# Kernel optimization log

Hardware: AMD Instinct MI355X
Metric: run time of the kernel (lower is better)

Reference implementation:

```python
import jax, jax.numpy as jnp
import numpy as np

B, S, D, H = 4, 2048, 1024, 16
DK = D // H


def setup_inputs() -> dict:
    key = jax.random.key(0)
    ks = jax.random.split(key, 12)
    s = 1.0 / np.sqrt(D)
    return {
        "query": jax.random.normal(ks[0], (B, S, D), jnp.float32),
        "key": jax.random.normal(ks[1], (B, S, D), jnp.float32),
        "value": jax.random.normal(ks[2], (B, S, D), jnp.float32),
        "mask": jnp.ones((1, 1, S, S), jnp.int32),
        "w_q": jax.random.normal(ks[3], (D, D), jnp.float32) * s,
        "b_q": jax.random.normal(ks[4], (D,), jnp.float32) * s,
        "w_k": jax.random.normal(ks[5], (D, D), jnp.float32) * s,
        "b_k": jax.random.normal(ks[6], (D,), jnp.float32) * s,
        "w_v": jax.random.normal(ks[7], (D, D), jnp.float32) * s,
        "b_v": jax.random.normal(ks[8], (D,), jnp.float32) * s,
        "w_o": jax.random.normal(ks[9], (D, D), jnp.float32) * s,
        "b_o": jax.random.normal(ks[10], (D,), jnp.float32) * s,
    }


def reference(query, key, value, mask, w_q, b_q, w_k, b_k, w_v, b_v, w_o, b_o):
    # linear projections (torch Linear: x @ W^T + b)
    q = query @ w_q.T + b_q
    k = key @ w_k.T + b_k
    v = value @ w_v.T + b_v
    # [B, S, D] -> [B, H, S, DK]
    q = q.reshape(B, S, H, DK).transpose(0, 2, 1, 3)
    k = k.reshape(B, S, H, DK).transpose(0, 2, 1, 3)
    v = v.reshape(B, S, H, DK).transpose(0, 2, 1, 3)
    scores = jnp.einsum("bhqd,bhkd->bhqk", q, k) / jnp.sqrt(jnp.float32(DK))
    scores = jnp.where(mask == 0, jnp.float32(-1e9), scores)
    attn = jax.nn.softmax(scores, axis=-1)  # dropout p=0.0 -> identity
    x = jnp.einsum("bhqk,bhkd->bhqd", attn, v)
    x = x.transpose(0, 2, 1, 3).reshape(B, S, D)
    return x @ w_o.T + b_o
```

## Files before the change

### kernel.cpp

```cpp
#include <hip/hip_runtime.h>
#include <stdint.h>

#define S_LEN 2048
#define NHEAD 16
#define DHEAD 64
#define DMODEL 1024
#define MROWS 8192

typedef unsigned short ushort_t;
typedef __attribute__((ext_vector_type(8))) __bf16 bf16x8;
typedef __attribute__((ext_vector_type(4))) float f32x4;

__device__ __forceinline__ float bf2f(ushort_t h) {
    union { unsigned int u; float f; } v; v.u = ((unsigned int)h) << 16; return v.f;
}
__device__ __forceinline__ ushort_t f2bf(float f) {
    union { float f; unsigned int u; } v; v.f = f;
    unsigned int u = v.u + 0x7fffu + ((v.u >> 16) & 1u);
    return (ushort_t)(u >> 16);
}

__device__ __forceinline__ void gload_lds16(const void* g, void* l)
{
    auto* g1 = reinterpret_cast<const __attribute__((address_space(1))) void*>(
        reinterpret_cast<uintptr_t>(g));
    auto* l3 = reinterpret_cast<__attribute__((address_space(3))) void*>(
        reinterpret_cast<uintptr_t>(l));
    __builtin_amdgcn_global_load_lds(g1, l3, 16, 0, 0);
}

__global__ void detect_dtype(const unsigned int* __restrict__ q, int* __restrict__ flag)
{
    __shared__ int cnt;
    if (threadIdx.x == 0) cnt = 0;
    __syncthreads();
    int c = 0;
    for (int i = 0; i < 8; ++i) {
        const unsigned int w = q[threadIdx.x * 8 + i];
        const unsigned int lo = w & 0xffffu;
        const unsigned int e = (lo >> 7) & 0xffu;
        if (lo == 0u || (e >= 96u && e <= 160u)) ++c;
    }
    atomicAdd(&cnt, c);
    __syncthreads();
    if (threadIdx.x == 0) flag[0] = (cnt < 400) ? 1 : 0;
}

__global__ void mask_flags(const int* __restrict__ mask, int* __restrict__ flags)
{
    __shared__ int ok_s;
    if (threadIdx.x == 0) ok_s = 1;
    __syncthreads();
    const int t = blockIdx.x;
    const int tq = t >> 4, tk = t & 15;
    int ok = 1;
    for (int i = 0; i < 64; ++i) {
        const int idx = i * 256 + threadIdx.x;
        const int r = idx >> 7, c = idx & 127;
        if (mask[(size_t)(tq * 128 + r) * S_LEN + tk * 128 + c] == 0) { ok = 0; break; }
    }
    if (!ok) atomicAnd(&ok_s, 0);
    __syncthreads();
    if (threadIdx.x == 0) flags[t] = ok_s;
}

__device__ __forceinline__ float loadscal(const void* b, int i, bool f32)
{
    return f32 ? ((const float*)b)[i] : bf2f(((const ushort_t*)b)[i]);
}

__global__ __launch_bounds__(256)
void conv_bf16(const void* __restrict__ src, ushort_t* __restrict__ dst,
               int n8, const int* __restrict__ dflag, int fidx)
{
    const bool f32 = dflag[fidx] != 0;
    const int stride = gridDim.x * 256;
    for (int i = blockIdx.x * 256 + threadIdx.x; i < n8; i += stride) {
        if (f32) {
            const float4 a = ((const float4*)src)[2 * (size_t)i];
            const float4 b = ((const float4*)src)[2 * (size_t)i + 1];
            union { ushort_t u[8]; uint4 v; } p;
            p.u[0] = f2bf(a.x); p.u[1] = f2bf(a.y); p.u[2] = f2bf(a.z); p.u[3] = f2bf(a.w);
            p.u[4] = f2bf(b.x); p.u[5] = f2bf(b.y); p.u[6] = f2bf(b.z); p.u[7] = f2bf(b.w);
            ((uint4*)dst)[i] = p.v;
        } else {
            ((uint4*)dst)[i] = ((const uint4*)src)[i];
        }
    }
}

template <bool OUTF>
__global__ __launch_bounds__(256, 2)
void gemm_bf16(const ushort_t* __restrict__ A, const ushort_t* __restrict__ W,
               const void* __restrict__ bias, void* __restrict__ out,
               const int* __restrict__ dflag)
{
    constexpr int K = DMODEL, N = DMODEL;
    __shared__ ushort_t As[3][128 * 32];
    __shared__ ushort_t Bs[3][128 * 32];
    const bool bf32 = dflag[1] != 0;
    const int tid = threadIdx.x;
    const int lane = tid & 63;
    const int wave = tid >> 6;
    const int lrow = lane & 15, lq = lane >> 4;
    const int m0 = blockIdx.x * 128;
    const int n0 = blockIdx.y * 128;
    const int wr = (wave >> 1) * 64;
    const int wc = (wave & 1) * 64;

    const f32x4 zero4 = {0.f, 0.f, 0.f, 0.f};
    f32x4 acc[4][4];
#pragma unroll
    for (int i = 0; i < 4; ++i)
#pragma unroll
        for (int j = 0; j < 4; ++j) acc[i][j] = zero4;

    const int r0  = tid >> 2;
    const int cc0 = (tid & 3) * 8;
    const int lb  = wave * 64 * 8;
    const int lb1 = (wave * 64 + 256) * 8;

    auto stage = [&](int buf, int k0) __attribute__((always_inline)) {
        gload_lds16(&A[(size_t)(m0 + r0) * K + k0 + cc0],      &As[buf][lb]);
        gload_lds16(&A[(size_t)(m0 + r0 + 64) * K + k0 + cc0], &As[buf][lb1]);
        gload_lds16(&W[(size_t)(n0 + r0) * K + k0 + cc0],      &Bs[buf][lb]);
        gload_lds16(&W[(size_t)(n0 + r0 + 64) * K + k0 + cc0], &Bs[buf][lb1]);
    };
    auto compute = [&](int buf) __attribute__((always_inline)) {
        bf16x8 af[4], bfr[4];
#pragma unroll
        for (int t = 0; t < 4; ++t) {
            af[t]  = *(const bf16x8*)(&As[buf][(wr + t * 16 + lrow) * 32 + lq * 8]);
            bfr[t] = *(const bf16x8*)(&Bs[buf][(wc + t * 16 + lrow) * 32 + lq * 8]);
        }
        __builtin_amdgcn_s_setprio(1);
#pragma unroll
        for (int mt = 0; mt < 4; ++mt)
#pragma unroll
            for (int nt = 0; nt < 4; ++nt)
                acc[mt][nt] = __builtin_amdgcn_mfma_f32_16x16x32_bf16(
                    af[mt], bfr[nt], acc[mt][nt], 0, 0, 0);
        __builtin_amdgcn_s_setprio(0);
    };

    stage(0, 0);
    stage(1, 32);
    asm volatile("s_waitcnt vmcnt(4)" ::: "memory");
    __builtin_amdgcn_s_barrier();

#pragma unroll 1
    for (int tt = 0; tt < 32; ++tt) {
        if (tt < 30) stage((tt + 2) % 3, (tt + 2) * 32);
        compute(tt % 3);
        if (tt < 31) {
            if (tt < 30) asm volatile("s_waitcnt vmcnt(4)" ::: "memory");
            else         asm volatile("s_waitcnt vmcnt(0)" ::: "memory");
            __builtin_amdgcn_s_barrier();
        }
    }

#pragma unroll
    for (int nt = 0; nt < 4; ++nt) {
        const int n = n0 + wc + nt * 16 + lrow;
        const float bv = loadscal(bias, n, bf32);
#pragma unroll
        for (int mt = 0; mt < 4; ++mt) {
            const int mbase = m0 + wr + mt * 16 + lq * 4;
#pragma unroll
            for (int r = 0; r < 4; ++r) {
                const float v = acc[mt][nt][r] + bv;
                const size_t o = (size_t)(mbase + r) * N + n;
                if (OUTF) ((float*)out)[o] = v;
                else      ((ushort_t*)out)[o] = f2bf(v);
            }
        }
    }
}

__global__ __launch_bounds__(256, 2)
void attn_mfma(const ushort_t* __restrict__ Q, const ushort_t* __restrict__ K,
               const ushort_t* __restrict__ V, const int* __restrict__ mask,
               const int* __restrict__ flags, ushort_t* __restrict__ X)
{
    constexpr int KP = 72;
    constexpr int VP = 130;
    constexpr int PP = 68;
    constexpr float CEXP = 0.18033688f;
    __shared__ ushort_t Ks[128 * KP];
    __shared__ ushort_t VTs[64 * VP];
    __shared__ ushort_t Ps[4][32 * PP];

    const int tid = threadIdx.x;
    const int lane = tid & 63;
    const int wave = tid >> 6;
    const int lrow = lane & 15, lq = lane >> 4;
    const int bh = blockIdx.y, b = bh >> 4, h = bh & 15;
    const int q0 = blockIdx.x * 128;
    const int qw = q0 + wave * 32;
    const int coff = h * 64;
    const size_t rowb = (size_t)b * S_LEN;

    bf16x8 qf[2][2];
#pragma unroll
    for (int mt = 0; mt < 2; ++mt)
#pragma unroll
        for (int ks = 0; ks < 2; ++ks)
            qf[mt][ks] = *(const bf16x8*)(
                &Q[(rowb + qw + mt * 16 + lrow) * DMODEL + coff + ks * 32 + lq * 8]);

    const f32x4 zero4 = {0.f, 0.f, 0.f, 0.f};
    f32x4 o[2][4];
    float mr[2][4], lr[2][4];
#pragma unroll
    for (int mt = 0; mt < 2; ++mt) {
#pragma unroll
        for (int nt = 0; nt < 4; ++nt) o[mt][nt] = zero4;
#pragma unroll
        for (int r = 0; r < 4; ++r) { mr[mt][r] = -1e30f; lr[mt][r] = 0.f; }
    }

    ushort_t* const pw = &Ps[wave][0];

    for (int kt = 0; kt < 16; ++kt) {
        const int k0 = kt * 128;
#pragma unroll
        for (int i = 0; i < 4; ++i) {
            const int c = tid + i * 256;
            const int r = c >> 3, cc = (c & 7) * 8;
            *(uint4*)(&Ks[r * KP + cc]) =
                *(const uint4*)(&K[(rowb + k0 + r) * DMODEL + coff + cc]);
        }
#pragma unroll
        for (int i = 0; i < 2; ++i) {
            const int c = tid + i * 256;
            const int k2 = c >> 3;
            const int cc = (c & 7) * 8;
            union { uint4 v; ushort_t u[8]; } a, bb;
            a.v  = *(const uint4*)(&V[(rowb + k0 + 2 * k2)     * DMODEL + coff + cc]);
            bb.v = *(const uint4*)(&V[(rowb + k0 + 2 * k2 + 1) * DMODEL + coff + cc]);
#pragma unroll
            for (int j = 0; j < 8; ++j) {
                const unsigned int pk = (unsigned int)a.u[j] | ((unsigned int)bb.u[j] << 16);
                *(unsigned int*)(&VTs[(cc + j) * VP + 2 * k2]) = pk;
            }
        }
        __syncthreads();

        f32x4 s[2][8];
#pragma unroll
        for (int mt = 0; mt < 2; ++mt)
#pragma unroll
            for (int nt = 0; nt < 8; ++nt) s[mt][nt] = zero4;
        __builtin_amdgcn_s_setprio(1);
#pragma unroll
        for (int nt = 0; nt < 8; ++nt) {
#pragma unroll
            for (int ks = 0; ks < 2; ++ks) {
                const bf16x8 kf = *(const bf16x8*)(&Ks[(nt * 16 + lrow) * KP + ks * 32 + lq * 8]);
                s[0][nt] = __builtin_amdgcn_mfma_f32_16x16x32_bf16(qf[0][ks], kf, s[0][nt], 0, 0, 0);
                s[1][nt] = __builtin_amdgcn_mfma_f32_16x16x32_bf16(qf[1][ks], kf, s[1][nt], 0, 0, 0);
            }
        }
        __builtin_amdgcn_s_setprio(0);

        if (!flags[blockIdx.x * 16 + kt]) {
            for (int mt = 0; mt < 2; ++mt)
                for (int nt = 0; nt < 8; ++nt)
                    for (int r = 0; r < 4; ++r) {
                        const int qi = qw + mt * 16 + lq * 4 + r;
                        const int ki = k0 + nt * 16 + lrow;
                        if (mask[(size_t)qi * S_LEN + ki] == 0) s[mt][nt][r] = -1e9f;
                    }
        }

#pragma unroll
        for (int mt = 0; mt < 2; ++mt) {
#pragma unroll
            for (int r = 0; r < 4; ++r) {
                float v = fmaxf(
                    fmaxf(fmaxf(s[mt][0][r], s[mt][1][r]), fmaxf(s[mt][2][r], s[mt][3][r])),
                    fmaxf(fmaxf(s[mt][4][r], s[mt][5][r]), fmaxf(s[mt][6][r], s[mt][7][r])));
#pragma unroll
                for (int off = 1; off < 16; off <<= 1) v = fmaxf(v, __shfl_xor(v, off, 64));
                const float mn = fmaxf(mr[mt][r], v);
                const float alpha = __builtin_amdgcn_exp2f((mr[mt][r] - mn) * CEXP);
                mr[mt][r] = mn;
                const float mnC = mn * CEXP;
                float rs = 0.f;
#pragma unroll
                for (int nt = 0; nt < 8; ++nt) {
                    const float p = __builtin_amdgcn_exp2f(fmaf(s[mt][nt][r], CEXP, -mnC));
                    s[mt][nt][r] = p;
                    rs += p;
                }
#pragma unroll
                for (int off = 1; off < 16; off <<= 1) rs += __shfl_xor(rs, off, 64);
                lr[mt][r] = lr[mt][r] * alpha + rs;
#pragma unroll
                for (int nt = 0; nt < 4; ++nt) o[mt][nt][r] *= alpha;
            }
        }

#pragma unroll
        for (int half = 0; half < 2; ++half) {
#pragma unroll
            for (int mt = 0; mt < 2; ++mt)
#pragma unroll
                for (int nt = 0; nt < 4; ++nt)
#pragma unroll
                    for (int r = 0; r < 4; ++r)
                        pw[(mt * 16 + lq * 4 + r) * PP + nt * 16 + lrow] =
                            f2bf(s[mt][half * 4 + nt][r]);
#pragma unroll
            for (int ks = 0; ks < 2; ++ks) {
                const bf16x8 pf0 = *(const bf16x8*)(&pw[lrow * PP + ks * 32 + lq * 8]);
                const bf16x8 pf1 = *(const bf16x8*)(&pw[(16 + lrow) * PP + ks * 32 + lq * 8]);
                const int kb = half * 64 + ks * 32;
                __builtin_amdgcn_s_setprio(1);
#pragma unroll
                for (int nt = 0; nt < 4; ++nt) {
                    const bf16x8 vf = *(const bf16x8*)(
                        &VTs[(nt * 16 + lrow) * VP + kb + lq * 8]);
                    o[0][nt] = __builtin_amdgcn_mfma_f32_16x16x32_bf16(pf0, vf, o[0][nt], 0, 0, 0);
                    o[1][nt] = __builtin_amdgcn_mfma_f32_16x16x32_bf16(pf1, vf, o[1][nt], 0, 0, 0);
                }
                __builtin_amdgcn_s_setprio(0);
            }
        }
        __syncthreads();
    }

#pragma unroll
    for (int mt = 0; mt < 2; ++mt) {
#pragma unroll
        for (int r = 0; r < 4; ++r) {
            const float inv = 1.f / lr[mt][r];
            const int si = qw + mt * 16 + lq * 4 + r;
#pragma unroll
            for (int nt = 0; nt < 4; ++nt) {
                const int dk = nt * 16 + lrow;
                X[(rowb + si) * DMODEL + coff + dk] = f2bf(o[mt][nt][r] * inv);
            }
        }
    }
}

extern "C" void kernel_launch(void* const* d_in, const int* in_sizes, int n_in,
                              void* d_out, int out_size, void* d_ws, size_t ws_size,
                              hipStream_t stream)
{
    const void* query = d_in[0];
    const void* key   = d_in[1];
    const void* value = d_in[2];
    const int*  mask  = (const int*)d_in[3];
    const void* w_q = d_in[4];
    const void* b_q = d_in[5];
    const void* w_k = d_in[6];
    const void* b_k = d_in[7];
    const void* w_v = d_in[8];
    const void* b_v = d_in[9];
    const void* w_o = d_in[10];
    const void* b_o = d_in[11];

    const size_t TEN = (size_t)MROWS * DMODEL;
    ushort_t* Kp = (ushort_t*)d_ws;
    ushort_t* Vp = Kp + TEN;
    ushort_t* Xp = Vp + TEN;
    int* dflag   = (int*)(Xp + TEN);
    int* flags   = dflag + 2;
    ushort_t* Qp = (ushort_t*)d_out;
    ushort_t* Ac = Qp + TEN;
    ushort_t* Wq_c = Vp;
    ushort_t* Wk_c = Vp + (size_t)DMODEL * DMODEL;
    ushort_t* Wv_c = Xp;
    ushort_t* Wo_c = Vp;

    const int WN8 = DMODEL * DMODEL / 8;
    const int AN8 = (int)(TEN / 8);

    detect_dtype<<<1, 64, 0, stream>>>((const unsigned int*)query, dflag + 0);
    detect_dtype<<<1, 64, 0, stream>>>((const unsigned int*)w_q,   dflag + 1);
    mask_flags<<<256, 256, 0, stream>>>(mask, flags);

    conv_bf16<<<512, 256, 0, stream>>>(w_q, Wq_c, WN8, dflag, 1);
    conv_bf16<<<512, 256, 0, stream>>>(w_k, Wk_c, WN8, dflag, 1);
    conv_bf16<<<512, 256, 0, stream>>>(w_v, Wv_c, WN8, dflag, 1);

    const dim3 gg(64, 8);
    conv_bf16<<<2048, 256, 0, stream>>>(query, Ac, AN8, dflag, 0);
    gemm_bf16<false><<<gg, 256, 0, stream>>>(Ac, Wq_c, b_q, Qp, dflag);
    conv_bf16<<<2048, 256, 0, stream>>>(key, Ac, AN8, dflag, 0);
    gemm_bf16<false><<<gg, 256, 0, stream>>>(Ac, Wk_c, b_k, Kp, dflag);
    conv_bf16<<<2048, 256, 0, stream>>>(value, Ac, AN8, dflag, 0);
    gemm_bf16<false><<<gg, 256, 0, stream>>>(Ac, Wv_c, b_v, Vp, dflag);

    attn_mfma<<<dim3(16, 64), 256, 0, stream>>>(Qp, Kp, Vp, mask, flags, Xp);

    conv_bf16<<<512, 256, 0, stream>>>(w_o, Wo_c, WN8, dflag, 1);
    gemm_bf16<true><<<gg, 256, 0, stream>>>(Xp, Wo_c, b_o, d_out, dflag);
}
```

Baseline: 538.0 us.

## Batch Q and K projections into one launch and drop setprio in attention

The Q and K projection GEMMs are merged into a single launch with a z dimension of 2, which doubles the grid so the GPU is filled better. Workspace buffers are remapped to fit both bf16 activation copies at once. The GEMM's launch bounds rise from 2 to 3 blocks per CU, and the output dtype becomes a runtime flag instead of a template parameter. The s_setprio calls around the MFMA loops in attention are removed. Risks include register spilling under the tighter occupancy bound and a small cost from the runtime output branch.

```diff
diff --git a/kernel.cpp b/kernel.cpp
--- a/kernel.cpp
+++ b/kernel.cpp
@@ -89,16 +89,13 @@
     }
 }
 
-template <bool OUTF>
-__global__ __launch_bounds__(256, 2)
-void gemm_bf16(const ushort_t* __restrict__ A, const ushort_t* __restrict__ W,
-               const void* __restrict__ bias, void* __restrict__ out,
-               const int* __restrict__ dflag)
+__device__ __forceinline__ void gemm_core(
+    const ushort_t* __restrict__ A, const ushort_t* __restrict__ W,
+    const void* __restrict__ bias, void* __restrict__ out,
+    bool bf32, bool outf,
+    ushort_t (&As)[3][128 * 32], ushort_t (&Bs)[3][128 * 32])
 {
     constexpr int K = DMODEL, N = DMODEL;
-    __shared__ ushort_t As[3][128 * 32];
-    __shared__ ushort_t Bs[3][128 * 32];
-    const bool bf32 = dflag[1] != 0;
     const int tid = threadIdx.x;
     const int lane = tid & 63;
     const int wave = tid >> 6;
@@ -170,11 +167,35 @@
             for (int r = 0; r < 4; ++r) {
                 const float v = acc[mt][nt][r] + bv;
                 const size_t o = (size_t)(mbase + r) * N + n;
-                if (OUTF) ((float*)out)[o] = v;
+                if (outf) ((float*)out)[o] = v;
                 else      ((ushort_t*)out)[o] = f2bf(v);
             }
         }
     }
+}
+
+__global__ __launch_bounds__(256, 3)
+void gemm_bf16(const ushort_t* __restrict__ A, const ushort_t* __restrict__ W,
+               const void* __restrict__ bias, void* __restrict__ out,
+               const int* __restrict__ dflag, int outf)
+{
+    __shared__ ushort_t As[3][128 * 32];
+    __shared__ ushort_t Bs[3][128 * 32];
+    gemm_core(A, W, bias, out, dflag[1] != 0, outf != 0, As, Bs);
+}
+
+__global__ __launch_bounds__(256, 3)
+void gemm_qk(const ushort_t* __restrict__ A0, const ushort_t* __restrict__ W0,
+             const void* __restrict__ b0, void* __restrict__ o0,
+             const ushort_t* __restrict__ A1, const ushort_t* __restrict__ W1,
+             const void* __restrict__ b1, void* __restrict__ o1,
+             const int* __restrict__ dflag)
+{
+    __shared__ ushort_t As[3][128 * 32];
+    __shared__ ushort_t Bs[3][128 * 32];
+    const bool z = blockIdx.z != 0;
+    gemm_core(z ? A1 : A0, z ? W1 : W0, z ? b1 : b0, z ? o1 : o0,
+              dflag[1] != 0, false, As, Bs);
 }
 
 __global__ __launch_bounds__(256, 2)
@@ -251,7 +272,6 @@
         for (int mt = 0; mt < 2; ++mt)
 #pragma unroll
             for (int nt = 0; nt < 8; ++nt) s[mt][nt] = zero4;
-        __builtin_amdgcn_s_setprio(1);
 #pragma unroll
         for (int nt = 0; nt < 8; ++nt) {
 #pragma unroll
@@ -261,7 +281,6 @@
                 s[1][nt] = __builtin_amdgcn_mfma_f32_16x16x32_bf16(qf[1][ks], kf, s[1][nt], 0, 0, 0);
             }
         }
-        __builtin_amdgcn_s_setprio(0);
 
         if (!flags[blockIdx.x * 16 + kt]) {
             for (int mt = 0; mt < 2; ++mt)
@@ -316,7 +335,6 @@
                 const bf16x8 pf0 = *(const bf16x8*)(&pw[lrow * PP + ks * 32 + lq * 8]);
                 const bf16x8 pf1 = *(const bf16x8*)(&pw[(16 + lrow) * PP + ks * 32 + lq * 8]);
                 const int kb = half * 64 + ks * 32;
-                __builtin_amdgcn_s_setprio(1);
 #pragma unroll
                 for (int nt = 0; nt < 4; ++nt) {
                     const bf16x8 vf = *(const bf16x8*)(
@@ -324,7 +342,6 @@
                     o[0][nt] = __builtin_amdgcn_mfma_f32_16x16x32_bf16(pf0, vf, o[0][nt], 0, 0, 0);
                     o[1][nt] = __builtin_amdgcn_mfma_f32_16x16x32_bf16(pf1, vf, o[1][nt], 0, 0, 0);
                 }
-                __builtin_amdgcn_s_setprio(0);
             }
         }
         __syncthreads();
@@ -363,19 +380,24 @@
     const void* b_o = d_in[11];
 
     const size_t TEN = (size_t)MROWS * DMODEL;
-    ushort_t* Kp = (ushort_t*)d_ws;
-    ushort_t* Vp = Kp + TEN;
-    ushort_t* Xp = Vp + TEN;
-    int* dflag   = (int*)(Xp + TEN);
+    const size_t WEL = (size_t)DMODEL * DMODEL;
+    ushort_t* W0 = (ushort_t*)d_ws;
+    ushort_t* W1 = W0 + TEN;
+    ushort_t* W2 = W1 + TEN;
+    int* dflag   = (int*)(W2 + TEN);
     int* flags   = dflag + 2;
-    ushort_t* Qp = (ushort_t*)d_out;
-    ushort_t* Ac = Qp + TEN;
-    ushort_t* Wq_c = Vp;
-    ushort_t* Wk_c = Vp + (size_t)DMODEL * DMODEL;
-    ushort_t* Wv_c = Xp;
-    ushort_t* Wo_c = Vp;
-
-    const int WN8 = DMODEL * DMODEL / 8;
+
+    ushort_t* AcQ = (ushort_t*)d_out;
+    ushort_t* AcK = AcQ + TEN;
+    ushort_t* AcV = AcQ;
+    ushort_t* Vp  = AcK;
+
+    ushort_t* Wq_c = W2;
+    ushort_t* Wk_c = W2 + WEL;
+    ushort_t* Wv_c = W2 + 2 * WEL;
+    ushort_t* Wo_c = W1;
+
+    const int WN8 = (int)(WEL / 8);
     const int AN8 = (int)(TEN / 8);
 
     detect_dtype<<<1, 64, 0, stream>>>((const unsigned int*)query, dflag + 0);
@@ -385,17 +407,17 @@
     conv_bf16<<<512, 256, 0, stream>>>(w_q, Wq_c, WN8, dflag, 1);
     conv_bf16<<<512, 256, 0, stream>>>(w_k, Wk_c, WN8, dflag, 1);
     conv_bf16<<<512, 256, 0, stream>>>(w_v, Wv_c, WN8, dflag, 1);
-
-    const dim3 gg(64, 8);
-    conv_bf16<<<2048, 256, 0, stream>>>(query, Ac, AN8, dflag, 0);
-    gemm_bf16<false><<<gg, 256, 0, stream>>>(Ac, Wq_c, b_q, Qp, dflag);
-    conv_bf16<<<2048, 256, 0, stream>>>(key, Ac, AN8, dflag, 0);
-    gemm_bf16<false><<<gg, 256, 0, stream>>>(Ac, Wk_c, b_k, Kp, dflag);
-    conv_bf16<<<2048, 256, 0, stream>>>(value, Ac, AN8, dflag, 0);
-    gemm_bf16<false><<<gg, 256, 0, stream>>>(Ac, Wv_c, b_v, Vp, dflag);
-
-    attn_mfma<<<dim3(16, 64), 256, 0, stream>>>(Qp, Kp, Vp, mask, flags, Xp);
+    conv_bf16<<<2048, 256, 0, stream>>>(query, AcQ, AN8, dflag, 0);
+    conv_bf16<<<2048, 256, 0, stream>>>(key,   AcK, AN8, dflag, 0);
+
+    gemm_qk<<<dim3(64, 8, 2), 256, 0, stream>>>(AcQ, Wq_c, b_q, W0,
+                                                AcK, Wk_c, b_k, W1, dflag);
+
+    conv_bf16<<<2048, 256, 0, stream>>>(value, AcV, AN8, dflag, 0);
+    gemm_bf16<<<dim3(64, 8), 256, 0, stream>>>(AcV, Wv_c, b_v, Vp, dflag, 0);
+
+    attn_mfma<<<dim3(16, 64), 256, 0, stream>>>(W0, W1, Vp, mask, flags, W2);
 
     conv_bf16<<<512, 256, 0, stream>>>(w_o, Wo_c, WN8, dflag, 1);
-    gemm_bf16<true><<<gg, 256, 0, stream>>>(Xp, Wo_c, b_o, d_out, dflag);
-}
+    gemm_bf16<<<dim3(64, 8), 256, 0, stream>>>(W2, Wo_c, b_o, d_out, dflag, 1);
+}
```

Result: no change. 541.0 us (+0.6%).
